# Performance work log

Measured on AMD Instinct MI355X. Metric: run time of the kernel, lower is better.

## Reference

```python
import jax, jax.numpy as jnp
import numpy as np


def setup_inputs() -> dict:
    key = jax.random.key(0)
    ks = jax.random.split(key, 7)
    B = 4096
    x = jax.random.normal(ks[0], (B, 1, 28, 28), dtype=jnp.float32)
    # conv1: Conv2d(1, 32, 3), conv2: Conv2d(32, 64, 3)
    w1 = jax.random.normal(ks[1], (32, 1, 3, 3), dtype=jnp.float32) * 0.1
    b1 = jax.random.normal(ks[2], (32,), dtype=jnp.float32) * 0.1
    w2 = jax.random.normal(ks[3], (64, 32, 3, 3), dtype=jnp.float32) * 0.05
    b2 = jax.random.normal(ks[4], (64,), dtype=jnp.float32) * 0.05
    # fc1: Linear(9216, 128), fc2: Linear(128, 10)
    fc1_w = jax.random.normal(ks[5], (128, 9216), dtype=jnp.float32) * 0.01
    fc1_b = jnp.zeros((128,), dtype=jnp.float32)
    fc2_w = jax.random.normal(ks[6], (10, 128), dtype=jnp.float32) * 0.05
    fc2_b = jnp.zeros((10,), dtype=jnp.float32)
    return {"x": x, "w1": w1, "b1": b1, "w2": w2, "b2": b2,
            "fc1_w": fc1_w, "fc1_b": fc1_b, "fc2_w": fc2_w, "fc2_b": fc2_b}


def _conv_valid(x, w, b):
    # The original FFTConv1d (flatten-to-1D FFT circular correlation + roll +
    # crop) is mathematically identical to valid cross-correlation (nn.Conv2d).
    y = jax.lax.conv_general_dilated(
        x, w, window_strides=(1, 1), padding="VALID",
        dimension_numbers=("NCHW", "OIHW", "NCHW"))
    return y + b[None, :, None, None]


def reference(x, w1, b1, w2, b2, fc1_w, fc1_b, fc2_w, fc2_b):
    h = jax.nn.relu(_conv_valid(x, w1, b1))        # [B,32,26,26]
    h = jax.nn.relu(_conv_valid(h, w2, b2))        # [B,64,24,24]
    B, C, H, W = h.shape
    h = h.reshape(B, C, H // 2, 2, W // 2, 2).max(axis=(3, 5))  # maxpool 2x2 -> [B,64,12,12]
    # dropout layers are identity at inference
    h = h.reshape(B, -1)                           # [B,9216], C-major like torch.flatten
    h = jax.nn.relu(h @ fc1_w.T + fc1_b)           # [B,128]
    logits = h @ fc2_w.T + fc2_b                   # [B,10]
    # original computes log_softmax but returns the pre-softmax logits
    return logits
```

## Files before the change

### kernel.cpp

```cpp
#include <hip/hip_runtime.h>
#include <hip/hip_bf16.h>
#include <string.h>

using short8 = __attribute__((ext_vector_type(8))) short;
using f32x4  = __attribute__((ext_vector_type(4))) float;

#define POOLN     9216
#define FC1N      128
#define WT2_ELEMS 18432
#define WT2_BYTES 36864
#define H1S_STRIDE 36
#define XS_STRIDE  29

#define GLL16(gp, lp) __builtin_amdgcn_global_load_lds( \
    (const __attribute__((address_space(1))) void*)(gp), \
    (__attribute__((address_space(3))) void*)(lp), 16, 0, 0)

static __device__ __forceinline__ unsigned short f2bf(float f) {
  unsigned int u = __builtin_bit_cast(unsigned int, f);
  unsigned int r = (u + 0x7FFFu + ((u >> 16) & 1u)) >> 16;
  return (unsigned short)r;
}

static __device__ __forceinline__ unsigned int pkbf(float lo, float hi) {
  __hip_bfloat162 h2 = __float22bfloat162_rn(make_float2(lo, hi));
  unsigned int r;
  memcpy(&r, &h2, sizeof(r));
  return r;
}

__global__ __launch_bounds__(256) void k_wt2(const float* __restrict__ w2,
    unsigned short* __restrict__ wt2) {
  int idx = blockIdx.x * 256 + threadIdx.x;
  if (idx >= WT2_ELEMS) return;
  int j = idx & 7;
  int l = (idx >> 3) & 63;
  int tn = idx >> 9;
  int tap = tn >> 2, n = tn & 3;
  int oc = n * 16 + (l & 15);
  int ic = (l >> 4) * 8 + j;
  wt2[idx] = f2bf(w2[oc * 288 + ic * 9 + tap]);
}

__global__ __launch_bounds__(256) void k_fw1t(const float* __restrict__ w,
    unsigned short* __restrict__ wt) {
  int c = blockIdx.x;
  __shared__ float row[9216];
  int t = threadIdx.x;
  const float* src = w + (size_t)c * 9216;
  for (int i = t; i < 9216; i += 256) row[i] = src[i];
  __syncthreads();
  unsigned short* dst = wt + (size_t)c * 9216;
  for (int k = t; k < 9216; k += 256) {
    int sp = k >> 6, oc = k & 63;
    dst[k] = f2bf(row[oc * 144 + sp]);
  }
}

__global__ __launch_bounds__(256, 2) void kc_fused(const float* __restrict__ x,
    const float* __restrict__ w1, const float* __restrict__ b1,
    const unsigned short* __restrict__ wt2, const float* __restrict__ b2,
    unsigned short* __restrict__ pooled) {
  int img = blockIdx.x;
  __shared__ float xs[28 * XS_STRIDE];
  __shared__ __align__(16) unsigned short h1s[676 * H1S_STRIDE];
  int t = threadIdx.x;
  int wv = t >> 6, ln = t & 63;

  const float* xp = x + (size_t)img * 784;
  for (int i = t; i < 784; i += 256) {
    int r = i / 28, c = i - r * 28;
    xs[r * XS_STRIDE + c] = xp[i];
  }

  int wvu = __builtin_amdgcn_readfirstlane(wv);
  float wr[8][9], br[8];
  #pragma unroll
  for (int o = 0; o < 8; ++o) {
    br[o] = b1[wvu * 8 + o];
    #pragma unroll
    for (int q = 0; q < 9; ++q) wr[o][q] = w1[(wvu * 8 + o) * 9 + q];
  }
  __syncthreads();

  if (ln < 52) {
    int half = (ln >= 26);
    int xcol = ln - half * 26;
    int y0 = half * 13;
    float win[3][3];
    #pragma unroll
    for (int c = 0; c < 3; ++c) {
      win[1][c] = xs[(y0 + 0) * XS_STRIDE + xcol + c];
      win[2][c] = xs[(y0 + 1) * XS_STRIDE + xcol + c];
    }
    #pragma unroll
    for (int i = 0; i < 13; ++i) {
      #pragma unroll
      for (int c = 0; c < 3; ++c) {
        win[0][c] = win[1][c];
        win[1][c] = win[2][c];
        win[2][c] = xs[(y0 + i + 2) * XS_STRIDE + xcol + c];
      }
      unsigned int packed[4];
      #pragma unroll
      for (int o = 0; o < 8; o += 2) {
        float s0 = br[o], s1 = br[o + 1];
        #pragma unroll
        for (int r = 0; r < 3; ++r)
          #pragma unroll
          for (int c = 0; c < 3; ++c) {
            s0 = fmaf(win[r][c], wr[o][r * 3 + c], s0);
            s1 = fmaf(win[r][c], wr[o + 1][r * 3 + c], s1);
          }
        packed[o >> 1] = pkbf(fmaxf(s0, 0.f), fmaxf(s1, 0.f));
      }
      int pos = (y0 + i) * 26 + xcol;
      uint4 v = {packed[0], packed[1], packed[2], packed[3]};
      *(uint4*)&h1s[pos * H1S_STRIDE + wv * 8] = v;
    }
  }
  __syncthreads();

  int col = ln & 15;
  int g = (ln >> 4) & 3;

  int abase[9];
  #pragma unroll
  for (int m = 0; m < 9; ++m) {
    int mt = wv * 9 + m;
    int pr = mt / 3, tc = mt - pr * 3;
    int y = 2 * pr + (col & 1);
    int xx = 8 * tc + (col >> 1);
    abase[m] = (y * 26 + xx) * (H1S_STRIDE * 2) + g * 16;
  }

  f32x4 acc[9][4];
  #pragma unroll
  for (int m = 0; m < 9; ++m)
    #pragma unroll
    for (int n = 0; n < 4; ++n)
      acc[m][n] = (f32x4){0.f, 0.f, 0.f, 0.f};

  const char* hsb = (const char*)h1s;
  #pragma unroll
  for (int tap = 0; tap < 9; ++tap) {
    int ky = tap / 3, kx = tap - ky * 3;
    int toff = (ky * 26 + kx) * (H1S_STRIDE * 2);
    short8 bf[4];
    #pragma unroll
    for (int n = 0; n < 4; ++n)
      bf[n] = *(const short8*)(wt2 + ((size_t)(tap * 4 + n) * 64 + ln) * 8);
    #pragma unroll
    for (int m = 0; m < 9; ++m) {
      union { short8 v; uint2 d[2]; } af;
      af.d[0] = *(const uint2*)(hsb + abase[m] + toff);
      af.d[1] = *(const uint2*)(hsb + abase[m] + toff + 8);
      #pragma unroll
      for (int n = 0; n < 4; ++n)
        acc[m][n] = __builtin_amdgcn_mfma_f32_16x16x32_bf16(af.v, bf[n], acc[m][n], 0, 0, 0);
    }
  }

  float bias[4];
  #pragma unroll
  for (int n = 0; n < 4; ++n) bias[n] = b2[n * 16 + col];
  unsigned short* pp = pooled + (size_t)img * POOLN;
  #pragma unroll
  for (int m = 0; m < 9; ++m) {
    int mt = wv * 9 + m;
    int pr = mt / 3, tc = mt - pr * 3;
    int sp = pr * 12 + tc * 4 + g;
    float rv[4];
    #pragma unroll
    for (int n = 0; n < 4; ++n) {
      f32x4 a = acc[m][n];
      float v = fmaxf(fmaxf(a[0], a[1]), fmaxf(a[2], a[3]));
      rv[n] = fmaxf(v + bias[n], 0.f);
    }
    unsigned int p01 = pkbf(rv[0], rv[1]);
    unsigned int p23 = pkbf(rv[2], rv[3]);
    unsigned short* pr0 = pp + sp * 64 + col;
    pr0[0]  = (unsigned short)p01;
    pr0[16] = (unsigned short)(p01 >> 16);
    pr0[32] = (unsigned short)p23;
    pr0[48] = (unsigned short)(p23 >> 16);
  }
}

__global__ __launch_bounds__(256) void k3_fc1_mfma(
    const unsigned short* __restrict__ a, const unsigned short* __restrict__ w,
    float* __restrict__ part, int nrpad) {
  __shared__ __align__(16) unsigned short As[2][4096];
  __shared__ __align__(16) unsigned short Bs[2][8192];
  int row0 = blockIdx.x * 64;
  int kbase = blockIdx.y * 2304;
  int t = threadIdx.x;
  int wv = t >> 6, l = t & 63;
  int rsub = l >> 3;
  int src_sw = ((l & 7) ^ rsub) << 4;

  const char* abase = (const char*)a + (size_t)row0 * 18432;
  const char* bbase = (const char*)w;

  auto stage = [&](int buf, int step) {
    size_t k0b = (size_t)(kbase + step * 64) * 2;
    #pragma unroll
    for (int i = 0; i < 2; ++i) {
      int c = wv * 2 + i;
      GLL16(abase + (size_t)(c * 8 + rsub) * 18432 + k0b + src_sw,
            (char*)As[buf] + c * 1024);
    }
    #pragma unroll
    for (int i = 0; i < 4; ++i) {
      int c = wv * 4 + i;
      GLL16(bbase + (size_t)(c * 8 + rsub) * 18432 + k0b + src_sw,
            (char*)Bs[buf] + c * 1024);
    }
  };

  int wm = wv >> 1, wn = wv & 1;
  int lr = l & 15, g2 = l >> 4;
  int rdxor = (lr & 7) << 4;

  f32x4 acc[2][4];
  #pragma unroll
  for (int mf = 0; mf < 2; ++mf)
    #pragma unroll
    for (int nf = 0; nf < 4; ++nf)
      acc[mf][nf] = (f32x4){0.f, 0.f, 0.f, 0.f};

  stage(0, 0);
  __syncthreads();
  for (int s = 0; s < 36; ++s) {
    int cur = s & 1;
    if (s < 35) stage(cur ^ 1, s + 1);
    const char* Ab = (const char*)As[cur];
    const char* Bb = (const char*)Bs[cur];
    #pragma unroll
    for (int ksub = 0; ksub < 2; ++ksub) {
      int koff = (ksub * 64 + g2 * 16) ^ rdxor;
      short8 af0 = *(const short8*)(Ab + (wm * 32 + lr) * 128 + koff);
      short8 af1 = *(const short8*)(Ab + (wm * 32 + 16 + lr) * 128 + koff);
      short8 bf[4];
      #pragma unroll
      for (int nf = 0; nf < 4; ++nf)
        bf[nf] = *(const short8*)(Bb + (wn * 64 + nf * 16 + lr) * 128 + koff);
      #pragma unroll
      for (int nf = 0; nf < 4; ++nf) {
        acc[0][nf] = __builtin_amdgcn_mfma_f32_16x16x32_bf16(af0, bf[nf], acc[0][nf], 0, 0, 0);
        acc[1][nf] = __builtin_amdgcn_mfma_f32_16x16x32_bf16(af1, bf[nf], acc[1][nf], 0, 0, 0);
      }
    }
    __syncthreads();
  }

  float* pp = part + (size_t)blockIdx.y * nrpad * 128 + (size_t)row0 * 128;
  #pragma unroll
  for (int mf = 0; mf < 2; ++mf)
    #pragma unroll
    for (int nf = 0; nf < 4; ++nf)
      #pragma unroll
      for (int rr = 0; rr < 4; ++rr) {
        int r = wm * 32 + mf * 16 + g2 * 4 + rr;
        int c = wn * 64 + nf * 16 + lr;
        pp[r * 128 + c] = acc[mf][nf][rr];
      }
}

__global__ __launch_bounds__(256) void k_red(const float* __restrict__ part,
    const float* __restrict__ bias, float* __restrict__ f1o, int nr, int nrpad) {
  int i = blockIdx.x * 256 + threadIdx.x;
  if (i >= nr * 128) return;
  size_t stride = (size_t)nrpad * 128;
  float s = part[i] + part[stride + i] + part[2 * stride + i] + part[3 * stride + i];
  f1o[i] = fmaxf(s + bias[i & 127], 0.f);
}

__global__ __launch_bounds__(256) void k4_fc2(const float* __restrict__ h,
    const float* __restrict__ w, const float* __restrict__ bias,
    float* __restrict__ out, int nr) {
  int idx = blockIdx.x * 256 + threadIdx.x;
  if (idx >= nr * 10) return;
  int b = idx / 10;
  int j = idx - b * 10;
  const float4* hp = (const float4*)(h + (size_t)b * 128);
  const float4* wp = (const float4*)(w + (size_t)j * 128);
  float s = 0.f;
  #pragma unroll
  for (int q = 0; q < 32; ++q) {
    float4 hv = hp[q];
    float4 wv = wp[q];
    s = fmaf(hv.x, wv.x, s);
    s = fmaf(hv.y, wv.y, s);
    s = fmaf(hv.z, wv.z, s);
    s = fmaf(hv.w, wv.w, s);
  }
  out[idx] = s + bias[j];
}

extern "C" void kernel_launch(void* const* d_in, const int* in_sizes, int n_in,
                              void* d_out, int out_size, void* d_ws, size_t ws_size,
                              hipStream_t stream) {
  const float* x   = (const float*)d_in[0];
  const float* w1  = (const float*)d_in[1];
  const float* b1  = (const float*)d_in[2];
  const float* w2  = (const float*)d_in[3];
  const float* b2  = (const float*)d_in[4];
  const float* fw1 = (const float*)d_in[5];
  const float* fb1 = (const float*)d_in[6];
  const float* fw2 = (const float*)d_in[7];
  const float* fb2 = (const float*)d_in[8];
  float* out = (float*)d_out;

  const int B = in_sizes[0] / 784;

  unsigned short* wt2 = (unsigned short*)d_ws;
  unsigned short* fw1t = (unsigned short*)((char*)d_ws + WT2_BYTES);
  const size_t carve = WT2_BYTES + (size_t)9216 * 128 * 2;
  char* base = (char*)d_ws + carve;
  size_t avail = (ws_size > carve) ? ws_size - carve : 0;
  const size_t per_img = (size_t)POOLN * 2 + 512 + 2048;
  int Bc = (int)(avail / per_img);
  if (Bc > B) Bc = B;
  Bc &= ~63;
  if (Bc < 64) Bc = 64;

  unsigned short* pooled = (unsigned short*)base;
  float* f1o = (float*)(base + (size_t)Bc * (POOLN * 2));
  float* part = (float*)(base + (size_t)Bc * (POOLN * 2 + 512));

  k_wt2<<<(WT2_ELEMS + 255) / 256, 256, 0, stream>>>(w2, wt2);
  k_fw1t<<<128, 256, 0, stream>>>(fw1, fw1t);

  for (int i0 = 0; i0 < B; i0 += Bc) {
    int nr = (B - i0 < Bc) ? (B - i0) : Bc;
    int mtiles = (nr + 63) / 64;
    int nrpad = mtiles * 64;
    kc_fused<<<nr, 256, 0, stream>>>(x + (size_t)i0 * 784, w1, b1, wt2, b2, pooled);
    k3_fc1_mfma<<<dim3(mtiles, 4), 256, 0, stream>>>(pooled, fw1t, part, nrpad);
    k_red<<<(nr * 128 + 255) / 256, 256, 0, stream>>>(part, fb1, f1o, nr, nrpad);
    k4_fc2<<<(nr * 10 + 255) / 256, 256, 0, stream>>>(f1o, fw2, fb2,
                                                      out + (size_t)i0 * 10, nr);
  }
}
```

Baseline: 156.0 us.

## Warp-specialize conv kernel into producer/consumer pipeline over eight images

Replaces the one-image-per-block fused conv kernel with a 512-thread block that processes eight images. Four producer waves compute conv1 into a double-buffered LDS tile while four consumer waves run the conv2 MFMA and pooling on the previous image, with one barrier per stage. Conv1 now reads the input straight from global memory instead of staging it in LDS. This is meant to overlap the scalar conv1 phase with the MFMA phase and cut per-block launch and setup overhead. In exchange it needs twice the LDS, launches far fewer blocks (occupancy and tail risk), and each wave group is idle while the other finishes.

```diff
diff --git a/kernel.cpp b/kernel.cpp
--- a/kernel.cpp
+++ b/kernel.cpp
@@ -10,7 +10,7 @@
 #define WT2_ELEMS 18432
 #define WT2_BYTES 36864
 #define H1S_STRIDE 36
-#define XS_STRIDE  29
+#define P_IMGS    8
 
 #define GLL16(gp, lp) __builtin_amdgcn_global_load_lds( \
     (const __attribute__((address_space(1))) void*)(gp), \
@@ -57,133 +57,136 @@
   }
 }
 
-__global__ __launch_bounds__(256, 2) void kc_fused(const float* __restrict__ x,
+__global__ __launch_bounds__(512, 2) void kc_pipe(const float* __restrict__ x,
     const float* __restrict__ w1, const float* __restrict__ b1,
     const unsigned short* __restrict__ wt2, const float* __restrict__ b2,
-    unsigned short* __restrict__ pooled) {
-  int img = blockIdx.x;
-  __shared__ float xs[28 * XS_STRIDE];
-  __shared__ __align__(16) unsigned short h1s[676 * H1S_STRIDE];
+    unsigned short* __restrict__ pooled, int nr) {
+  __shared__ __align__(16) unsigned short h1s[2][676 * H1S_STRIDE];
   int t = threadIdx.x;
-  int wv = t >> 6, ln = t & 63;
-
-  const float* xp = x + (size_t)img * 784;
-  for (int i = t; i < 784; i += 256) {
-    int r = i / 28, c = i - r * 28;
-    xs[r * XS_STRIDE + c] = xp[i];
-  }
-
-  int wvu = __builtin_amdgcn_readfirstlane(wv);
-  float wr[8][9], br[8];
-  #pragma unroll
-  for (int o = 0; o < 8; ++o) {
-    br[o] = b1[wvu * 8 + o];
-    #pragma unroll
-    for (int q = 0; q < 9; ++q) wr[o][q] = w1[(wvu * 8 + o) * 9 + q];
-  }
-  __syncthreads();
-
-  if (ln < 52) {
-    int half = (ln >= 26);
-    int xcol = ln - half * 26;
-    int y0 = half * 13;
-    float win[3][3];
-    #pragma unroll
-    for (int c = 0; c < 3; ++c) {
-      win[1][c] = xs[(y0 + 0) * XS_STRIDE + xcol + c];
-      win[2][c] = xs[(y0 + 1) * XS_STRIDE + xcol + c];
-    }
-    #pragma unroll
-    for (int i = 0; i < 13; ++i) {
-      #pragma unroll
-      for (int c = 0; c < 3; ++c) {
-        win[0][c] = win[1][c];
-        win[1][c] = win[2][c];
-        win[2][c] = xs[(y0 + i + 2) * XS_STRIDE + xcol + c];
-      }
-      unsigned int packed[4];
-      #pragma unroll
-      for (int o = 0; o < 8; o += 2) {
-        float s0 = br[o], s1 = br[o + 1];
-        #pragma unroll
-        for (int r = 0; r < 3; ++r)
-          #pragma unroll
-          for (int c = 0; c < 3; ++c) {
-            s0 = fmaf(win[r][c], wr[o][r * 3 + c], s0);
-            s1 = fmaf(win[r][c], wr[o + 1][r * 3 + c], s1);
-          }
-        packed[o >> 1] = pkbf(fmaxf(s0, 0.f), fmaxf(s1, 0.f));
-      }
-      int pos = (y0 + i) * 26 + xcol;
-      uint4 v = {packed[0], packed[1], packed[2], packed[3]};
-      *(uint4*)&h1s[pos * H1S_STRIDE + wv * 8] = v;
-    }
-  }
-  __syncthreads();
+  int w = t >> 6, ln = t & 63;
+  int ibase = blockIdx.x * P_IMGS;
+  int navail = nr - ibase;
+  int n = navail < P_IMGS ? navail : P_IMGS;
+
+  int half = (ln >= 26);
+  int xcol = ln - half * 26;
+  int y0 = half * 13;
 
   int col = ln & 15;
   int g = (ln >> 4) & 3;
-
-  int abase[9];
-  #pragma unroll
-  for (int m = 0; m < 9; ++m) {
-    int mt = wv * 9 + m;
-    int pr = mt / 3, tc = mt - pr * 3;
-    int y = 2 * pr + (col & 1);
-    int xx = 8 * tc + (col >> 1);
-    abase[m] = (y * 26 + xx) * (H1S_STRIDE * 2) + g * 16;
-  }
-
-  f32x4 acc[9][4];
-  #pragma unroll
-  for (int m = 0; m < 9; ++m)
-    #pragma unroll
-    for (int n = 0; n < 4; ++n)
-      acc[m][n] = (f32x4){0.f, 0.f, 0.f, 0.f};
-
-  const char* hsb = (const char*)h1s;
-  #pragma unroll
-  for (int tap = 0; tap < 9; ++tap) {
-    int ky = tap / 3, kx = tap - ky * 3;
-    int toff = (ky * 26 + kx) * (H1S_STRIDE * 2);
-    short8 bf[4];
-    #pragma unroll
-    for (int n = 0; n < 4; ++n)
-      bf[n] = *(const short8*)(wt2 + ((size_t)(tap * 4 + n) * 64 + ln) * 8);
-    #pragma unroll
-    for (int m = 0; m < 9; ++m) {
-      union { short8 v; uint2 d[2]; } af;
-      af.d[0] = *(const uint2*)(hsb + abase[m] + toff);
-      af.d[1] = *(const uint2*)(hsb + abase[m] + toff + 8);
-      #pragma unroll
-      for (int n = 0; n < 4; ++n)
-        acc[m][n] = __builtin_amdgcn_mfma_f32_16x16x32_bf16(af.v, bf[n], acc[m][n], 0, 0, 0);
+  int wq = w - 4;
+
+  for (int p = 0; p <= n; ++p) {
+    asm volatile("" ::: "memory");
+    int cb = p & 1;
+    if (w < 4) {
+      if (p < n && ln < 52) {
+        float wr[8][9], br[8];
+        #pragma unroll
+        for (int o = 0; o < 8; ++o) {
+          br[o] = b1[w * 8 + o];
+          #pragma unroll
+          for (int q = 0; q < 9; ++q) wr[o][q] = w1[(w * 8 + o) * 9 + q];
+        }
+        const float* xg = x + (size_t)(ibase + p) * 784;
+        float win[3][3];
+        #pragma unroll
+        for (int c = 0; c < 3; ++c) {
+          win[1][c] = xg[y0 * 28 + xcol + c];
+          win[2][c] = xg[(y0 + 1) * 28 + xcol + c];
+        }
+        #pragma unroll
+        for (int i = 0; i < 13; ++i) {
+          #pragma unroll
+          for (int c = 0; c < 3; ++c) {
+            win[0][c] = win[1][c];
+            win[1][c] = win[2][c];
+            win[2][c] = xg[(y0 + i + 2) * 28 + xcol + c];
+          }
+          unsigned int packed[4];
+          #pragma unroll
+          for (int o = 0; o < 8; o += 2) {
+            float s0 = br[o], s1 = br[o + 1];
+            #pragma unroll
+            for (int r = 0; r < 3; ++r)
+              #pragma unroll
+              for (int c = 0; c < 3; ++c) {
+                s0 = fmaf(win[r][c], wr[o][r * 3 + c], s0);
+                s1 = fmaf(win[r][c], wr[o + 1][r * 3 + c], s1);
+              }
+            packed[o >> 1] = pkbf(fmaxf(s0, 0.f), fmaxf(s1, 0.f));
+          }
+          int pos = (y0 + i) * 26 + xcol;
+          unsigned short* dst = &h1s[cb][pos * H1S_STRIDE + w * 8];
+          *(uint2*)dst = make_uint2(packed[0], packed[1]);
+          *(uint2*)(dst + 4) = make_uint2(packed[2], packed[3]);
+        }
+      }
+    } else {
+      if (p >= 1) {
+        const char* hsb = (const char*)h1s[cb ^ 1];
+        int abase[9];
+        #pragma unroll
+        for (int m = 0; m < 9; ++m) {
+          int mt = wq * 9 + m;
+          int pr = mt / 3, tc = mt - pr * 3;
+          int y = 2 * pr + (col & 1);
+          int xx = 8 * tc + (col >> 1);
+          abase[m] = (y * 26 + xx) * (H1S_STRIDE * 2) + g * 16;
+        }
+        f32x4 acc[9][4];
+        #pragma unroll
+        for (int m = 0; m < 9; ++m)
+          #pragma unroll
+          for (int nn = 0; nn < 4; ++nn)
+            acc[m][nn] = (f32x4){0.f, 0.f, 0.f, 0.f};
+
+        #pragma unroll
+        for (int tap = 0; tap < 9; ++tap) {
+          int ky = tap / 3, kx = tap - ky * 3;
+          int toff = (ky * 26 + kx) * (H1S_STRIDE * 2);
+          short8 bf[4];
+          #pragma unroll
+          for (int nn = 0; nn < 4; ++nn)
+            bf[nn] = *(const short8*)(wt2 + ((size_t)(tap * 4 + nn) * 64 + ln) * 8);
+          #pragma unroll
+          for (int m = 0; m < 9; ++m) {
+            union { short8 v; uint2 d[2]; } af;
+            af.d[0] = *(const uint2*)(hsb + abase[m] + toff);
+            af.d[1] = *(const uint2*)(hsb + abase[m] + toff + 8);
+            #pragma unroll
+            for (int nn = 0; nn < 4; ++nn)
+              acc[m][nn] = __builtin_amdgcn_mfma_f32_16x16x32_bf16(af.v, bf[nn], acc[m][nn], 0, 0, 0);
+          }
+        }
+
+        float bias[4];
+        #pragma unroll
+        for (int nn = 0; nn < 4; ++nn) bias[nn] = b2[nn * 16 + col];
+        unsigned short* pp = pooled + (size_t)(ibase + p - 1) * POOLN;
+        #pragma unroll
+        for (int m = 0; m < 9; ++m) {
+          int mt = wq * 9 + m;
+          int pr = mt / 3, tc = mt - pr * 3;
+          int sp = pr * 12 + tc * 4 + g;
+          float rv[4];
+          #pragma unroll
+          for (int nn = 0; nn < 4; ++nn) {
+            f32x4 a = acc[m][nn];
+            float v = fmaxf(fmaxf(a[0], a[1]), fmaxf(a[2], a[3]));
+            rv[nn] = fmaxf(v + bias[nn], 0.f);
+          }
+          unsigned int p01 = pkbf(rv[0], rv[1]);
+          unsigned int p23 = pkbf(rv[2], rv[3]);
+          unsigned short* pr0 = pp + sp * 64 + col;
+          pr0[0]  = (unsigned short)p01;
+          pr0[16] = (unsigned short)(p01 >> 16);
+          pr0[32] = (unsigned short)p23;
+          pr0[48] = (unsigned short)(p23 >> 16);
+        }
+      }
     }
-  }
-
-  float bias[4];
-  #pragma unroll
-  for (int n = 0; n < 4; ++n) bias[n] = b2[n * 16 + col];
-  unsigned short* pp = pooled + (size_t)img * POOLN;
-  #pragma unroll
-  for (int m = 0; m < 9; ++m) {
-    int mt = wv * 9 + m;
-    int pr = mt / 3, tc = mt - pr * 3;
-    int sp = pr * 12 + tc * 4 + g;
-    float rv[4];
-    #pragma unroll
-    for (int n = 0; n < 4; ++n) {
-      f32x4 a = acc[m][n];
-      float v = fmaxf(fmaxf(a[0], a[1]), fmaxf(a[2], a[3]));
-      rv[n] = fmaxf(v + bias[n], 0.f);
-    }
-    unsigned int p01 = pkbf(rv[0], rv[1]);
-    unsigned int p23 = pkbf(rv[2], rv[3]);
-    unsigned short* pr0 = pp + sp * 64 + col;
-    pr0[0]  = (unsigned short)p01;
-    pr0[16] = (unsigned short)(p01 >> 16);
-    pr0[32] = (unsigned short)p23;
-    pr0[48] = (unsigned short)(p23 >> 16);
+    __syncthreads();
   }
 }
 
@@ -336,7 +339,9 @@
     int nr = (B - i0 < Bc) ? (B - i0) : Bc;
     int mtiles = (nr + 63) / 64;
     int nrpad = mtiles * 64;
-    kc_fused<<<nr, 256, 0, stream>>>(x + (size_t)i0 * 784, w1, b1, wt2, b2, pooled);
+    int nblk = (nr + P_IMGS - 1) / P_IMGS;
+    kc_pipe<<<nblk, 512, 0, stream>>>(x + (size_t)i0 * 784, w1, b1, wt2, b2,
+                                      pooled, nr);
     k3_fc1_mfma<<<dim3(mtiles, 4), 256, 0, stream>>>(pooled, fw1t, part, nrpad);
     k_red<<<(nr * 128 + 255) / 256, 256, 0, stream>>>(part, fb1, f1o, nr, nrpad);
     k4_fc2<<<(nr * 10 + 255) / 256, 256, 0, stream>>>(f1o, fw2, fb2,
```

Result: slower. 425.6 us (+172.7%).

## Split fused conv kernel into three row tiles per image for occupancy

Applied to the files above, without the earlier changes.

The fused conv1+conv2+pool kernel now processes each image as three blocks of 8 output rows (grid y=3) instead of one block per image. Each block computes conv1 for 10 rows plus halo into smaller LDS, and each wave holds 3 instead of 9 MFMA accumulator tiles. This cuts registers and LDS per block so launch bounds can request 3 blocks per CU, raising parallelism. In exchange, the conv1 halo rows are recomputed across tiles and the conv2 weights are loaded three times per image.

```diff
diff --git a/kernel.cpp b/kernel.cpp
--- a/kernel.cpp
+++ b/kernel.cpp
@@ -57,20 +57,22 @@
   }
 }
 
-__global__ __launch_bounds__(256, 2) void kc_fused(const float* __restrict__ x,
+__global__ __launch_bounds__(256, 3) void kc_fused(const float* __restrict__ x,
     const float* __restrict__ w1, const float* __restrict__ b1,
     const unsigned short* __restrict__ wt2, const float* __restrict__ b2,
     unsigned short* __restrict__ pooled) {
   int img = blockIdx.x;
-  __shared__ float xs[28 * XS_STRIDE];
-  __shared__ __align__(16) unsigned short h1s[676 * H1S_STRIDE];
+  int tt = blockIdx.y;
+  __shared__ float xs[12 * XS_STRIDE];
+  __shared__ __align__(16) unsigned short h1s[260 * H1S_STRIDE];
   int t = threadIdx.x;
   int wv = t >> 6, ln = t & 63;
-
-  const float* xp = x + (size_t)img * 784;
-  for (int i = t; i < 784; i += 256) {
+  int r0x = tt * 8;
+
+  const float* xp = x + (size_t)img * 784 + (size_t)r0x * 28;
+  for (int i = t; i < 12 * 28; i += 256) {
     int r = i / 28, c = i - r * 28;
-    xs[r * XS_STRIDE + c] = xp[i];
+    xs[r * XS_STRIDE + c] = xp[r * 28 + c];
   }
 
   int wvu = __builtin_amdgcn_readfirstlane(wv);
@@ -86,7 +88,7 @@
   if (ln < 52) {
     int half = (ln >= 26);
     int xcol = ln - half * 26;
-    int y0 = half * 13;
+    int y0 = half * 5;
     float win[3][3];
     #pragma unroll
     for (int c = 0; c < 3; ++c) {
@@ -94,7 +96,7 @@
       win[2][c] = xs[(y0 + 1) * XS_STRIDE + xcol + c];
     }
     #pragma unroll
-    for (int i = 0; i < 13; ++i) {
+    for (int i = 0; i < 5; ++i) {
       #pragma unroll
       for (int c = 0; c < 3; ++c) {
         win[0][c] = win[1][c];
@@ -115,8 +117,9 @@
         packed[o >> 1] = pkbf(fmaxf(s0, 0.f), fmaxf(s1, 0.f));
       }
       int pos = (y0 + i) * 26 + xcol;
-      uint4 v = {packed[0], packed[1], packed[2], packed[3]};
-      *(uint4*)&h1s[pos * H1S_STRIDE + wv * 8] = v;
+      unsigned short* dst = &h1s[pos * H1S_STRIDE + wv * 8];
+      *(uint2*)dst = make_uint2(packed[0], packed[1]);
+      *(uint2*)(dst + 4) = make_uint2(packed[2], packed[3]);
     }
   }
   __syncthreads();
@@ -124,19 +127,17 @@
   int col = ln & 15;
   int g = (ln >> 4) & 3;
 
-  int abase[9];
-  #pragma unroll
-  for (int m = 0; m < 9; ++m) {
-    int mt = wv * 9 + m;
-    int pr = mt / 3, tc = mt - pr * 3;
-    int y = 2 * pr + (col & 1);
-    int xx = 8 * tc + (col >> 1);
-    abase[m] = (y * 26 + xx) * (H1S_STRIDE * 2) + g * 16;
-  }
-
-  f32x4 acc[9][4];
-  #pragma unroll
-  for (int m = 0; m < 9; ++m)
+  int abase[3];
+  #pragma unroll
+  for (int i = 0; i < 3; ++i) {
+    int y = 2 * wv + (col & 1);
+    int xx = 8 * i + (col >> 1);
+    abase[i] = (y * 26 + xx) * (H1S_STRIDE * 2) + g * 16;
+  }
+
+  f32x4 acc[3][4];
+  #pragma unroll
+  for (int m = 0; m < 3; ++m)
     #pragma unroll
     for (int n = 0; n < 4; ++n)
       acc[m][n] = (f32x4){0.f, 0.f, 0.f, 0.f};
@@ -151,7 +152,7 @@
     for (int n = 0; n < 4; ++n)
       bf[n] = *(const short8*)(wt2 + ((size_t)(tap * 4 + n) * 64 + ln) * 8);
     #pragma unroll
-    for (int m = 0; m < 9; ++m) {
+    for (int m = 0; m < 3; ++m) {
       union { short8 v; uint2 d[2]; } af;
       af.d[0] = *(const uint2*)(hsb + abase[m] + toff);
       af.d[1] = *(const uint2*)(hsb + abase[m] + toff + 8);
@@ -165,11 +166,10 @@
   #pragma unroll
   for (int n = 0; n < 4; ++n) bias[n] = b2[n * 16 + col];
   unsigned short* pp = pooled + (size_t)img * POOLN;
-  #pragma unroll
-  for (int m = 0; m < 9; ++m) {
-    int mt = wv * 9 + m;
-    int pr = mt / 3, tc = mt - pr * 3;
-    int sp = pr * 12 + tc * 4 + g;
+  int pr = tt * 4 + wv;
+  #pragma unroll
+  for (int m = 0; m < 3; ++m) {
+    int sp = pr * 12 + m * 4 + g;
     float rv[4];
     #pragma unroll
     for (int n = 0; n < 4; ++n) {
@@ -336,7 +336,8 @@
     int nr = (B - i0 < Bc) ? (B - i0) : Bc;
     int mtiles = (nr + 63) / 64;
     int nrpad = mtiles * 64;
-    kc_fused<<<nr, 256, 0, stream>>>(x + (size_t)i0 * 784, w1, b1, wt2, b2, pooled);
+    kc_fused<<<dim3(nr, 3), 256, 0, stream>>>(x + (size_t)i0 * 784, w1, b1,
+                                              wt2, b2, pooled);
     k3_fc1_mfma<<<dim3(mtiles, 4), 256, 0, stream>>>(pooled, fw1t, part, nrpad);
     k_red<<<(nr * 128 + 255) / 256, 256, 0, stream>>>(part, fb1, f1o, nr, nrpad);
     k4_fc2<<<(nr * 10 + 255) / 256, 256, 0, stream>>>(f1o, fw2, fb2,
```

Result: no change. 157.9 us (+1.2%).
